# Optimization experiments

Measured on AMD Instinct MI355X. Metric: run time of the kernel, lower is better.

## Reference

```python
import jax, jax.numpy as jnp
import numpy as np

D_MODEL = 1024
N_HEADS = 16
HEAD_DIM = D_MODEL // N_HEADS
B, S = 4, 2048
NEG = -1000000000.0


def setup_inputs() -> dict:
    key = jax.random.key(0)
    ks = jax.random.split(key, 13)
    sc = 1.0 / np.sqrt(D_MODEL)
    return {
        "query": jax.random.normal(ks[0], (B, S, D_MODEL), jnp.float32),
        "key": jax.random.normal(ks[1], (B, S, D_MODEL), jnp.float32),
        "value": jax.random.normal(ks[2], (B, S, D_MODEL), jnp.float32),
        "mask": jax.random.randint(ks[3], (B, 1, 1, S), 0, 2, jnp.int32),
        "Wq": jax.random.normal(ks[4], (D_MODEL, D_MODEL), jnp.float32) * sc,
        "bq": jax.random.normal(ks[5], (D_MODEL,), jnp.float32) * sc,
        "Wk": jax.random.normal(ks[6], (D_MODEL, D_MODEL), jnp.float32) * sc,
        "bk": jax.random.normal(ks[7], (D_MODEL,), jnp.float32) * sc,
        "Wv": jax.random.normal(ks[8], (D_MODEL, D_MODEL), jnp.float32) * sc,
        "bv": jax.random.normal(ks[9], (D_MODEL,), jnp.float32) * sc,
        "Wo": jax.random.normal(ks[10], (D_MODEL, D_MODEL), jnp.float32) * sc,
        "bo": jax.random.normal(ks[11], (D_MODEL,), jnp.float32) * sc,
    }


def _split_heads(x):
    b, s, _ = x.shape
    return x.reshape(b, s, N_HEADS, HEAD_DIM).transpose(0, 2, 1, 3)  # (B,H,S,Dh)


def reference(query, key, value, mask, Wq, bq, Wk, bk, Wv, bv, Wo, bo):
    # torch Linear: y = x @ W.T + b
    Q = _split_heads(query @ Wq.T + bq)
    K = _split_heads(key @ Wk.T + bk)
    V = _split_heads(value @ Wv.T + bv)
    scores = jnp.einsum("bhqd,bhkd->bhqk", Q, K) / np.sqrt(HEAD_DIM)
    scores = jnp.where(mask == 0, NEG, scores)
    probs = jax.nn.softmax(scores, axis=-1)
    ctx = jnp.einsum("bhqk,bhkd->bhqd", probs, V)
    ctx = ctx.transpose(0, 2, 1, 3).reshape(query.shape[0], query.shape[1], D_MODEL)
    return ctx @ Wo.T + bo
```

## Files before the change

kernel.cpp:

```cpp
#include <hip/hip_runtime.h>


typedef __bf16 bf16x8 __attribute__((ext_vector_type(8)));
typedef __bf16 bf16x4 __attribute__((ext_vector_type(4)));
typedef float  f32x4  __attribute__((ext_vector_type(4)));

#define LOG2E 1.44269504088896340736f
#define SCALE_Q (0.125f * LOG2E)
#define MBIAS_L2 (-1.44269504e9f)
#define MFMA16(a, b, c) __builtin_amdgcn_mfma_f32_16x16x32_bf16(a, b, c, 0, 0, 0)

__device__ inline unsigned short f2bf(float f) {
  unsigned int u = __float_as_uint(f);
  u = u + 0x7FFF + ((u >> 16) & 1);
  return (unsigned short)(u >> 16);
}
__device__ inline void gload16(const void* g, void* l) {
  __builtin_amdgcn_global_load_lds(
      (const __attribute__((address_space(1))) void*)g,
      (__attribute__((address_space(3))) void*)l, 16, 0, 0);
}
__device__ inline bf16x8 cvt8(const float* p) {
  float4 a = *(const float4*)p, b = *(const float4*)(p + 4);
  bf16x8 v;
  v[0] = (__bf16)a.x; v[1] = (__bf16)a.y; v[2] = (__bf16)a.z; v[3] = (__bf16)a.w;
  v[4] = (__bf16)b.x; v[5] = (__bf16)b.y; v[6] = (__bf16)b.z; v[7] = (__bf16)b.w;
  return v;
}

struct CvtJob { const float* s; unsigned short* d; int n8; };
struct CvtJobs { CvtJob j[8]; };
__global__ void cvt_all(CvtJobs J) {
  CvtJob jb = J.j[blockIdx.y];
  int i = blockIdx.x * 256 + threadIdx.x;
  if (blockIdx.y == 7) {
    if (i < jb.n8) {
      int4 m = ((const int4*)jb.s)[i];
      float4 o;
      o.x = m.x ? 0.f : MBIAS_L2;
      o.y = m.y ? 0.f : MBIAS_L2;
      o.z = m.z ? 0.f : MBIAS_L2;
      o.w = m.w ? 0.f : MBIAS_L2;
      ((float4*)jb.d)[i] = o;
    }
    return;
  }
  if (i < jb.n8) *(bf16x8*)(jb.d + (size_t)i * 8) = cvt8(jb.s + (size_t)i * 8);
}

struct ProjJob { const unsigned short* A; const unsigned short* W;
                 const float* bias; unsigned short* out; float scale; };
struct ProjJobs { ProjJob j[3]; };

__global__ __launch_bounds__(256, 2) void gemm_qkv(ProjJobs J) {
  __shared__ __align__(16) unsigned short Al[2][128 * 32];
  __shared__ __align__(16) unsigned short Wl[2][128 * 32];
  const int z = blockIdx.z;
  const ProjJob jb = J.j[z];
  const int tid = threadIdx.x, lane = tid & 63, w = tid >> 6;
  const int lid = lane & 15, lg = lane >> 4;
  const int lin = blockIdx.x + 8 * (int)blockIdx.y;
  const int xcd = lin & 7, j = lin >> 3;
  const int c0 = (j & 7) * 128;
  const int t0 = ((j >> 3) * 8 + xcd) * 128;
  const int wm = (w & 1) * 64, wn = (w >> 1) * 64;

  f32x4 acc[4][4];
#pragma unroll
  for (int i = 0; i < 4; i++)
#pragma unroll
    for (int jj = 0; jj < 4; jj++) acc[i][jj] = (f32x4){0.f, 0.f, 0.f, 0.f};

  auto stage = [&](int bi, int kt) {
#pragma unroll
    for (int i = 0; i < 2; i++) {
      int c = i * 256 + tid, r = c >> 2, ko = (c & 3) * 8;
      gload16(jb.A + (size_t)(t0 + r) * 1024 + kt + ko, &Al[bi][c * 8]);
      gload16(jb.W + (size_t)(c0 + r) * 1024 + kt + ko, &Wl[bi][c * 8]);
    }
  };
  auto compute = [&](int bi) {
    const unsigned short* Ml = (z == 2) ? Al[bi] : Wl[bi];
    const unsigned short* Nl = (z == 2) ? Wl[bi] : Al[bi];
    bf16x8 mf[4], nf[4];
#pragma unroll
    for (int mi = 0; mi < 4; mi++)
      mf[mi] = *(const bf16x8*)(&Ml[(wm + mi * 16 + lid) * 32 + lg * 8]);
#pragma unroll
    for (int ni = 0; ni < 4; ni++)
      nf[ni] = *(const bf16x8*)(&Nl[(wn + ni * 16 + lid) * 32 + lg * 8]);
#pragma unroll
    for (int mi = 0; mi < 4; mi++)
#pragma unroll
      for (int ni = 0; ni < 4; ni++)
        acc[mi][ni] = MFMA16(mf[mi], nf[ni], acc[mi][ni]);
  };

  stage(0, 0);
  __syncthreads();
  for (int kt = 0; kt < 1024; kt += 64) {
    stage(1, kt + 32);
    compute(0);
    __syncthreads();
    if (kt + 64 < 1024) stage(0, kt + 64);
    compute(1);
    __syncthreads();
  }

  if (z < 2) {
    const float scale = jb.scale;
#pragma unroll
    for (int mi = 0; mi < 4; mi++) {
      int colb = c0 + wm + mi * 16 + lg * 4;
      float4 b4 = *(const float4*)(&jb.bias[colb]);
#pragma unroll
      for (int ni = 0; ni < 4; ni++) {
        int token = t0 + wn + ni * 16 + lid;
        ushort4 st;
        st.x = f2bf((acc[mi][ni][0] + b4.x) * scale);
        st.y = f2bf((acc[mi][ni][1] + b4.y) * scale);
        st.z = f2bf((acc[mi][ni][2] + b4.z) * scale);
        st.w = f2bf((acc[mi][ni][3] + b4.w) * scale);
        *(ushort4*)(&jb.out[(size_t)token * 1024 + colb]) = st;
      }
    }
  } else {
    const int b = t0 >> 11;
#pragma unroll
    for (int ni = 0; ni < 4; ni++) {
      int col = c0 + wn + ni * 16 + lid;
      int h = col >> 6, d = col & 63;
      float bv = jb.bias[col];
#pragma unroll
      for (int mi = 0; mi < 4; mi++) {
        int s = (t0 & 2047) + wm + mi * 16 + lg * 4;
        ushort4 st;
        st.x = f2bf(acc[mi][ni][0] + bv);
        st.y = f2bf(acc[mi][ni][1] + bv);
        st.z = f2bf(acc[mi][ni][2] + bv);
        st.w = f2bf(acc[mi][ni][3] + bv);
        *(ushort4*)(&jb.out[(size_t)((b * 16 + h) * 64 + d) * 2048 + s]) = st;
      }
    }
  }
}

__global__ __launch_bounds__(256, 2) void gemm_o(
    const unsigned short* __restrict__ A, const unsigned short* __restrict__ W,
    const float* __restrict__ bias, float* __restrict__ C) {
  __shared__ __align__(16) unsigned short Al[2][128 * 32];
  __shared__ __align__(16) unsigned short Wl[2][128 * 32];
  const int tid = threadIdx.x, lane = tid & 63, w = tid >> 6;
  const int lid = lane & 15, lg = lane >> 4;
  const int lin = blockIdx.x + 8 * (int)blockIdx.y;
  const int xcd = lin & 7, j = lin >> 3;
  const int c0 = (j & 7) * 128;
  const int t0 = ((j >> 3) * 8 + xcd) * 128;
  const int wc = (w & 1) * 64, wt = (w >> 1) * 64;
  f32x4 acc[4][4];
#pragma unroll
  for (int i = 0; i < 4; i++)
#pragma unroll
    for (int jj = 0; jj < 4; jj++) acc[i][jj] = (f32x4){0.f, 0.f, 0.f, 0.f};

  auto stage = [&](int bi, int kt) {
#pragma unroll
    for (int i = 0; i < 2; i++) {
      int c = i * 256 + tid, r = c >> 2, ko = (c & 3) * 8;
      gload16(A + (size_t)(t0 + r) * 1024 + kt + ko, &Al[bi][c * 8]);
      gload16(W + (size_t)(c0 + r) * 1024 + kt + ko, &Wl[bi][c * 8]);
    }
  };
  auto compute = [&](int bi) {
    bf16x8 aw[4], bt[4];
#pragma unroll
    for (int mi = 0; mi < 4; mi++)
      aw[mi] = *(const bf16x8*)(&Wl[bi][(wc + mi * 16 + lid) * 32 + lg * 8]);
#pragma unroll
    for (int ni = 0; ni < 4; ni++)
      bt[ni] = *(const bf16x8*)(&Al[bi][(wt + ni * 16 + lid) * 32 + lg * 8]);
#pragma unroll
    for (int mi = 0; mi < 4; mi++)
#pragma unroll
      for (int ni = 0; ni < 4; ni++)
        acc[mi][ni] = MFMA16(aw[mi], bt[ni], acc[mi][ni]);
  };

  stage(0, 0);
  __syncthreads();
  for (int kt = 0; kt < 1024; kt += 64) {
    stage(1, kt + 32);
    compute(0);
    __syncthreads();
    if (kt + 64 < 1024) stage(0, kt + 64);
    compute(1);
    __syncthreads();
  }
#pragma unroll
  for (int mi = 0; mi < 4; mi++) {
    int colb = c0 + wc + mi * 16 + lg * 4;
    float4 b4 = *(const float4*)(&bias[colb]);
#pragma unroll
    for (int ni = 0; ni < 4; ni++) {
      int token = t0 + wt + ni * 16 + lid;
      float4 st;
      st.x = acc[mi][ni][0] + b4.x;
      st.y = acc[mi][ni][1] + b4.y;
      st.z = acc[mi][ni][2] + b4.z;
      st.w = acc[mi][ni][3] + b4.w;
      *(float4*)(&C[(size_t)token * 1024 + colb]) = st;
    }
  }
}

__global__ __launch_bounds__(256, 4) void attn(
    const unsigned short* __restrict__ Qp,
    const unsigned short* __restrict__ Kp,
    const unsigned short* __restrict__ Vt,
    const float* __restrict__ mbias,
    unsigned short* __restrict__ ctx) {
  __shared__ __align__(16) unsigned short Klds[2][64 * 64];
  __shared__ __align__(16) unsigned short Vlds[2][64 * 64];

  const int tid = threadIdx.x, lane = tid & 63, w = tid >> 6;
  const int lid = lane & 15, lg = lane >> 4;
  const int wg = blockIdx.x + (int)(gridDim.x) * blockIdx.y;
  const int xcd = wg & 7, idx = wg >> 3;
  const int bh = (xcd << 3) | (idx >> 4);
  const int q0 = (idx & 15) * 128;
  const int b = bh >> 4, h = bh & 15;
  const int wq = w * 32;
  const int x7 = lid & 7;

  const unsigned short* Kg = Kp + (size_t)(b * 2048) * 1024 + h * 64;
  const unsigned short* Vg = Vt + (size_t)bh * 64 * 2048;
  const float* mg = mbias + b * 2048;

  bf16x8 qf[2][2];
#pragma unroll
  for (int qt = 0; qt < 2; qt++)
#pragma unroll
    for (int ks = 0; ks < 2; ks++) {
      int qrow = b * 2048 + q0 + wq + qt * 16 + lid;
      qf[qt][ks] = *(const bf16x8*)(Qp + (size_t)qrow * 1024 + h * 64 + ks * 32 + lg * 8);
    }

  f32x4 Ot[4][2];
#pragma unroll
  for (int dt = 0; dt < 4; dt++)
#pragma unroll
    for (int qt = 0; qt < 2; qt++) Ot[dt][qt] = (f32x4){0.f, 0.f, 0.f, 0.f};
  f32x4 acc_l[2] = {(f32x4){0.f, 0.f, 0.f, 0.f}, (f32x4){0.f, 0.f, 0.f, 0.f}};
  bf16x8 ones8;
#pragma unroll
  for (int i = 0; i < 8; i++) ones8[i] = (__bf16)1.0f;

  auto stage_kv = [&](unsigned short* Kl, unsigned short* Vl, int k0) {
#pragma unroll
    for (int i = 0; i < 2; i++) {
      int c = i * 256 + tid, r = c >> 3, gsw = (c & 7) ^ (r & 7);
      gload16(Kg + (size_t)(k0 + r) * 1024 + gsw * 8, Kl + c * 8);
    }
#pragma unroll
    for (int i = 0; i < 2; i++) {
      int c = i * 256 + tid, d = c >> 3, gsw = (c & 7) ^ (d & 7);
      gload16(Vg + (size_t)d * 2048 + k0 + gsw * 8, Vl + c * 8);
    }
  };

  auto qk_half = [&](int kt, const unsigned short* Kl, int qt, f32x4 (&accS)[4]) {
    const float* mrow = mg + kt * 64;
#pragma unroll
    for (int mt = 0; mt < 4; mt++)
      accS[mt] = *(const f32x4*)(&mrow[mt * 16 + lg * 4]);
    __builtin_amdgcn_s_setprio(1);
#pragma unroll
    for (int ks = 0; ks < 2; ks++) {
      int koff = ((ks * 4 + lg) ^ x7) * 8;
#pragma unroll
      for (int mt = 0; mt < 4; mt++) {
        bf16x8 a = *(const bf16x8*)(&Kl[(mt * 16 + lid) * 64 + koff]);
        accS[mt] = MFMA16(a, qf[qt][ks], accS[mt]);
      }
    }
    __builtin_amdgcn_s_setprio(0);
  };

  auto sm_half = [&](f32x4 (&accS)[4], bf16x8 (&pb)[2]) {
#pragma unroll
    for (int mt = 0; mt < 4; mt++) {
      int half = (mt & 1) * 4;
#pragma unroll
      for (int r = 0; r < 4; r++) {
        float p = __builtin_amdgcn_exp2f(accS[mt][r]);
        pb[mt >> 1][half + r] = (__bf16)p;
      }
    }
  };

  auto pv_joint = [&](bf16x8 (&pb0)[2], bf16x8 (&pb1)[2], const unsigned short* Vl) {
    __builtin_amdgcn_s_setprio(1);
#pragma unroll
    for (int c = 0; c < 2; c++) {
      acc_l[0] = MFMA16(ones8, pb0[c], acc_l[0]);
      acc_l[1] = MFMA16(ones8, pb1[c], acc_l[1]);
    }
#pragma unroll
    for (int c = 0; c < 2; c++) {
      int glo = ((4 * c + (lg >> 1)) ^ x7) * 8 + (lg & 1) * 4;
      int ghi = ((4 * c + 2 + (lg >> 1)) ^ x7) * 8 + (lg & 1) * 4;
#pragma unroll
      for (int dt = 0; dt < 4; dt++) {
        const unsigned short* vrow = &Vl[(dt * 16 + lid) * 64];
        bf16x4 lo = *(const bf16x4*)(&vrow[glo]);
        bf16x4 hi = *(const bf16x4*)(&vrow[ghi]);
        bf16x8 av = __builtin_shufflevector(lo, hi, 0, 1, 2, 3, 4, 5, 6, 7);
        Ot[dt][0] = MFMA16(av, pb0[c], Ot[dt][0]);
        Ot[dt][1] = MFMA16(av, pb1[c], Ot[dt][1]);
      }
    }
    __builtin_amdgcn_s_setprio(0);
  };

  auto compute_tile = [&](const unsigned short* Kl, const unsigned short* Vl, int kt) {
    f32x4 accS[4];
    bf16x8 pb0[2], pb1[2];
    qk_half(kt, Kl, 0, accS);
    sm_half(accS, pb0);
    qk_half(kt, Kl, 1, accS);
    sm_half(accS, pb1);
    pv_joint(pb0, pb1, Vl);
  };

  stage_kv(&Klds[0][0], &Vlds[0][0], 0);
  __syncthreads();

  for (int kt = 0; kt < 32; kt += 2) {
    stage_kv(&Klds[1][0], &Vlds[1][0], (kt + 1) * 64);
    compute_tile(&Klds[0][0], &Vlds[0][0], kt);
    __syncthreads();
    if (kt + 2 < 32) stage_kv(&Klds[0][0], &Vlds[0][0], (kt + 2) * 64);
    compute_tile(&Klds[1][0], &Vlds[1][0], kt + 1);
    __syncthreads();
  }

#pragma unroll
  for (int qt = 0; qt < 2; qt++) {
    float inv = 1.0f / acc_l[qt][0];
    int qrow = b * 2048 + q0 + wq + qt * 16 + lid;
#pragma unroll
    for (int dt = 0; dt < 4; dt++) {
      ushort4 st;
      st.x = f2bf(Ot[dt][qt][0] * inv);
      st.y = f2bf(Ot[dt][qt][1] * inv);
      st.z = f2bf(Ot[dt][qt][2] * inv);
      st.w = f2bf(Ot[dt][qt][3] * inv);
      *(ushort4*)(&ctx[(size_t)qrow * 1024 + h * 64 + dt * 16 + lg * 4]) = st;
    }
  }
}

extern "C" void kernel_launch(void* const* d_in, const int* in_sizes, int n_in,
                              void* d_out, int out_size, void* d_ws, size_t ws_size,
                              hipStream_t stream) {
  const float* q  = (const float*)d_in[0];
  const float* k  = (const float*)d_in[1];
  const float* v  = (const float*)d_in[2];
  const int*   mk = (const int*)d_in[3];
  const float* Wq = (const float*)d_in[4];
  const float* bq = (const float*)d_in[5];
  const float* Wk = (const float*)d_in[6];
  const float* bk = (const float*)d_in[7];
  const float* Wv = (const float*)d_in[8];
  const float* bv = (const float*)d_in[9];
  const float* Wo = (const float*)d_in[10];
  const float* bo = (const float*)d_in[11];

  const size_t NTOK = (size_t)8192 * 1024;
  const size_t NW = (size_t)1024 * 1024;

  unsigned short* qb  = (unsigned short*)d_ws;
  unsigned short* kb  = qb + NTOK;
  unsigned short* vb  = kb + NTOK;
  unsigned short* Qp  = vb + NTOK;
  unsigned short* Kp  = Qp + NTOK;
  unsigned short* Vt  = Kp + NTOK;
  unsigned short* Wqb = Vt + NTOK;
  unsigned short* Wkb = Wqb + NW;
  unsigned short* Wvb = Wkb + NW;
  unsigned short* Wob = Wvb + NW;
  float*          mbg = (float*)(Wob + NW);
  unsigned short* ctx = qb;

  CvtJobs J;
  J.j[0] = {q, qb, (int)(NTOK / 8)};
  J.j[1] = {k, kb, (int)(NTOK / 8)};
  J.j[2] = {v, vb, (int)(NTOK / 8)};
  J.j[3] = {Wq, Wqb, (int)(NW / 8)};
  J.j[4] = {Wk, Wkb, (int)(NW / 8)};
  J.j[5] = {Wv, Wvb, (int)(NW / 8)};
  J.j[6] = {Wo, Wob, (int)(NW / 8)};
  J.j[7] = {(const float*)mk, (unsigned short*)mbg, 2048};
  cvt_all<<<dim3(4096, 8), 256, 0, stream>>>(J);

  ProjJobs P;
  P.j[0] = {qb, Wqb, bq, Qp, SCALE_Q};
  P.j[1] = {kb, Wkb, bk, Kp, 1.0f};
  P.j[2] = {vb, Wvb, bv, Vt, 1.0f};
  gemm_qkv<<<dim3(8, 64, 3), 256, 0, stream>>>(P);

  attn<<<dim3(16, 64), 256, 0, stream>>>(Qp, Kp, Vt, mbg, ctx);
  gemm_o<<<dim3(8, 64), 256, 0, stream>>>(ctx, Wob, bo, (float*)d_out);
}
```

Measured before the change: 338.6 us.

## Permute V layout in projection epilogue and share K fragments across query tiles

The V projection epilogue now writes the sequence index in a permuted order inside each 32-element group. This lets the attention PV loop read one contiguous 8-element bf16 vector per lane instead of two 4-element reads and a shuffle. The QK step is also merged across both query tiles, so each K fragment read from LDS feeds two MFMAs instead of being read twice. In exchange the score accumulators for both tiles are live at once, which raises register pressure and couples the V layout to the consumer's access pattern.

After: 336.0 us. No clear change (-0.8%).

```diff
diff --git a/kernel.cpp b/kernel.cpp
--- a/kernel.cpp
+++ b/kernel.cpp
@@ -134,12 +134,13 @@
 #pragma unroll
       for (int mi = 0; mi < 4; mi++) {
         int s = (t0 & 2047) + wm + mi * 16 + lg * 4;
+        int sp = (s & ~31) | (((s >> 2) & 3) << 3) | (((s >> 4) & 1) << 2);
         ushort4 st;
         st.x = f2bf(acc[mi][ni][0] + bv);
         st.y = f2bf(acc[mi][ni][1] + bv);
         st.z = f2bf(acc[mi][ni][2] + bv);
         st.w = f2bf(acc[mi][ni][3] + bv);
-        *(ushort4*)(&jb.out[(size_t)((b * 16 + h) * 64 + d) * 2048 + s]) = st;
+        *(ushort4*)(&jb.out[(size_t)((b * 16 + h) * 64 + d) * 2048 + sp]) = st;
       }
     }
   }
@@ -268,11 +269,15 @@
     }
   };
 
-  auto qk_half = [&](int kt, const unsigned short* Kl, int qt, f32x4 (&accS)[4]) {
+  auto compute_tile = [&](const unsigned short* Kl, const unsigned short* Vl, int kt) {
     const float* mrow = mg + kt * 64;
-#pragma unroll
-    for (int mt = 0; mt < 4; mt++)
-      accS[mt] = *(const f32x4*)(&mrow[mt * 16 + lg * 4]);
+    f32x4 accS[4][2];
+#pragma unroll
+    for (int mt = 0; mt < 4; mt++) {
+      f32x4 mb4 = *(const f32x4*)(&mrow[mt * 16 + lg * 4]);
+      accS[mt][0] = mb4;
+      accS[mt][1] = mb4;
+    }
     __builtin_amdgcn_s_setprio(1);
 #pragma unroll
     for (int ks = 0; ks < 2; ks++) {
@@ -280,56 +285,43 @@
 #pragma unroll
       for (int mt = 0; mt < 4; mt++) {
         bf16x8 a = *(const bf16x8*)(&Kl[(mt * 16 + lid) * 64 + koff]);
-        accS[mt] = MFMA16(a, qf[qt][ks], accS[mt]);
+        accS[mt][0] = MFMA16(a, qf[0][ks], accS[mt][0]);
+        accS[mt][1] = MFMA16(a, qf[1][ks], accS[mt][1]);
       }
     }
     __builtin_amdgcn_s_setprio(0);
-  };
-
-  auto sm_half = [&](f32x4 (&accS)[4], bf16x8 (&pb)[2]) {
-#pragma unroll
-    for (int mt = 0; mt < 4; mt++) {
-      int half = (mt & 1) * 4;
-#pragma unroll
-      for (int r = 0; r < 4; r++) {
-        float p = __builtin_amdgcn_exp2f(accS[mt][r]);
-        pb[mt >> 1][half + r] = (__bf16)p;
+
+    bf16x8 pb[2][2];
+#pragma unroll
+    for (int qt = 0; qt < 2; qt++)
+#pragma unroll
+      for (int mt = 0; mt < 4; mt++) {
+        int half = (mt & 1) * 4;
+#pragma unroll
+        for (int r = 0; r < 4; r++) {
+          float p = __builtin_amdgcn_exp2f(accS[mt][qt][r]);
+          pb[mt >> 1][qt][half + r] = (__bf16)p;
+        }
       }
-    }
-  };
-
-  auto pv_joint = [&](bf16x8 (&pb0)[2], bf16x8 (&pb1)[2], const unsigned short* Vl) {
+
     __builtin_amdgcn_s_setprio(1);
 #pragma unroll
+    for (int c = 0; c < 2; c++)
+#pragma unroll
+      for (int qt = 0; qt < 2; qt++)
+        acc_l[qt] = MFMA16(ones8, pb[c][qt], acc_l[qt]);
+
+#pragma unroll
     for (int c = 0; c < 2; c++) {
-      acc_l[0] = MFMA16(ones8, pb0[c], acc_l[0]);
-      acc_l[1] = MFMA16(ones8, pb1[c], acc_l[1]);
-    }
-#pragma unroll
-    for (int c = 0; c < 2; c++) {
-      int glo = ((4 * c + (lg >> 1)) ^ x7) * 8 + (lg & 1) * 4;
-      int ghi = ((4 * c + 2 + (lg >> 1)) ^ x7) * 8 + (lg & 1) * 4;
+      int goff = (((c * 4 + lg) ^ x7)) * 8;
 #pragma unroll
       for (int dt = 0; dt < 4; dt++) {
-        const unsigned short* vrow = &Vl[(dt * 16 + lid) * 64];
-        bf16x4 lo = *(const bf16x4*)(&vrow[glo]);
-        bf16x4 hi = *(const bf16x4*)(&vrow[ghi]);
-        bf16x8 av = __builtin_shufflevector(lo, hi, 0, 1, 2, 3, 4, 5, 6, 7);
-        Ot[dt][0] = MFMA16(av, pb0[c], Ot[dt][0]);
-        Ot[dt][1] = MFMA16(av, pb1[c], Ot[dt][1]);
+        bf16x8 av = *(const bf16x8*)(&Vl[(dt * 16 + lid) * 64 + goff]);
+        Ot[dt][0] = MFMA16(av, pb[c][0], Ot[dt][0]);
+        Ot[dt][1] = MFMA16(av, pb[c][1], Ot[dt][1]);
       }
     }
     __builtin_amdgcn_s_setprio(0);
-  };
-
-  auto compute_tile = [&](const unsigned short* Kl, const unsigned short* Vl, int kt) {
-    f32x4 accS[4];
-    bf16x8 pb0[2], pb1[2];
-    qk_half(kt, Kl, 0, accS);
-    sm_half(accS, pb0);
-    qk_half(kt, Kl, 1, accS);
-    sm_half(accS, pb1);
-    pv_joint(pb0, pb1, Vl);
   };
 
   stage_kv(&Klds[0][0], &Vlds[0][0], 0);
```
